# Kernel optimization log

Hardware: AMD Instinct MI355X
Metric: run time of the kernel (lower is better)

Reference implementation:

```python
import jax, jax.numpy as jnp
from jax import lax
import numpy as np

N, C, T, V, P, O = 32, 64, 300, 25, 3, 128
STRIDE = 2
EPS = 1e-5


def setup_inputs() -> dict:
    key = jax.random.key(0)
    ks = jax.random.split(key, 8)
    x = jax.random.normal(ks[0], (N, C, T, V), jnp.float32)
    A_parts = jax.random.uniform(ks[1], (P, V, V), jnp.float32)
    edge_importance = jnp.ones((P,), jnp.float32)
    gcn_w = jax.random.normal(ks[2], (O, C), jnp.float32) * 0.05
    gcn_b = jax.random.normal(ks[3], (O,), jnp.float32) * 0.05
    tcn_w = jax.random.normal(ks[4], (O, O, 9, 1), jnp.float32) * 0.02
    tcn_b = jax.random.normal(ks[5], (O,), jnp.float32) * 0.05
    bn_gamma = jnp.ones((O,), jnp.float32)
    bn_beta = jnp.zeros((O,), jnp.float32)
    res_w = jax.random.normal(ks[6], (O, C), jnp.float32) * 0.05
    res_b = jax.random.normal(ks[7], (O,), jnp.float32) * 0.05
    return {"x": x, "A_parts": A_parts, "edge_importance": edge_importance,
            "gcn_w": gcn_w, "gcn_b": gcn_b, "tcn_w": tcn_w, "tcn_b": tcn_b,
            "bn_gamma": bn_gamma, "bn_beta": bn_beta, "res_w": res_w, "res_b": res_b}


def reference(x, A_parts, edge_importance, gcn_w, gcn_b, tcn_w, tcn_b,
              bn_gamma, bn_beta, res_w, res_b):
    # Fused P-partition aggregation: sum_p (ei_p * A_p) applied once.
    A_sum = jnp.einsum('pvw,p->vw', A_parts, edge_importance)  # [V, V]
    agg = jnp.einsum('nctv,vw->nctw', x, A_sum)                # [N, C, T, V]
    # 1x1 gcn conv == channel matmul
    x_gcn = jnp.einsum('nctv,oc->notv', agg, gcn_w) + gcn_b[None, :, None, None]
    # temporal conv: kernel (9,1), stride (2,1), pad (4,0)
    x_tcn = lax.conv_general_dilated(
        x_gcn, tcn_w, window_strides=(STRIDE, 1), padding=((4, 4), (0, 0)),
        dimension_numbers=('NCHW', 'OIHW', 'NCHW'))
    x_tcn = x_tcn + tcn_b[None, :, None, None]
    # BatchNorm (training mode: batch statistics, biased variance)
    mean = jnp.mean(x_tcn, axis=(0, 2, 3), keepdims=True)
    var = jnp.var(x_tcn, axis=(0, 2, 3), keepdims=True)
    x_bn = (x_tcn - mean) * lax.rsqrt(var + EPS)
    x_bn = x_bn * bn_gamma[None, :, None, None] + bn_beta[None, :, None, None]
    # residual: 1x1 conv, stride (2,1) == temporal subsample + channel matmul
    x_sub = x[:, :, ::STRIDE, :]
    res = jnp.einsum('nctv,oc->notv', x_sub, res_w) + res_b[None, :, None, None]
    return jax.nn.relu(x_bn + res)
```

## Files before the change

kernel.cpp:

```cpp
#include <hip/hip_runtime.h>
#include <hip/hip_bf16.h>

typedef unsigned short u16;
typedef unsigned int   u32;

#define NB 32
#define CC 64
#define TT 300
#define VV 25
#define OO 128
#define TO 150
#define KT 9
#define MM 7500
#define MT 59
#define M2 3750

typedef short s8v  __attribute__((ext_vector_type(8)));
typedef float f4v  __attribute__((ext_vector_type(4)));
typedef u16  h4v  __attribute__((ext_vector_type(4)));
typedef u16  h8v  __attribute__((ext_vector_type(8)));

__device__ __forceinline__ float b2f(u16 u){
  union { u32 i; float f; } c; c.i = ((u32)u) << 16; return c.f;
}
__device__ __forceinline__ u16 f2b(float f){
  __hip_bfloat16 h = __float2bfloat16(f);
  return *reinterpret_cast<u16*>(&h);
}
__device__ __forceinline__ void async16(const void* g, void* l){
  __builtin_amdgcn_global_load_lds((const __attribute__((address_space(1))) u32*)g,
                                   (__attribute__((address_space(3))) u32*)l, 16, 0, 0);
}

__global__ __launch_bounds__(256) void k_prep(const float* __restrict__ Ap, const float* __restrict__ ei,
                                              const float* __restrict__ tw, const float* __restrict__ gw,
                                              const float* __restrict__ rw,
                                              float* __restrict__ Asum, float* __restrict__ zbuf,
                                              u16* __restrict__ Wq2, u16* __restrict__ gwb,
                                              u16* __restrict__ rwb){
  int idx = blockIdx.x * 256 + threadIdx.x;
  if (idx < VV*VV){
    float s = 0.f;
    for (int p = 0; p < 3; ++p) s += ei[p] * Ap[p*VV*VV + idx];
    Asum[idx] = s;
  }
  if (idx >= 640 && idx < 768) zbuf[idx - 640] = 0.f;
  int w = idx - 1024;
  if (w >= 0 && w < 18*OO*64){
    int kc = w >> 13;
    int r  = w & 8191;
    int o  = r >> 6;
    int j  = r & 63;
    int k  = kc >> 1;
    int i  = (kc & 1)*64 + j;
    Wq2[w] = f2b(tw[o*(OO*KT) + i*KT + k]);
  }
  int w2 = idx - 148480;
  if (w2 >= 0 && w2 < OO*CC) gwb[w2] = f2b(gw[w2]);
  int w3 = idx - 156672;
  if (w3 >= 0 && w3 < OO*CC) rwb[w3] = f2b(rw[w3]);
}

__global__ __launch_bounds__(256, 4) void k_gcnm(const float* __restrict__ x, const float* __restrict__ Asum,
                                                 const u16* __restrict__ gwb, const float* __restrict__ gb,
                                                 u16* __restrict__ xg){
  __shared__ __align__(16) u16 A_lds[128*64];
  __shared__ __align__(16) u16 B_lds[128*64];
  int bx = blockIdx.x;
  int n  = bx / MT;
  int m0 = (bx % MT) * 128;
  int t0 = m0 / VV, r0 = m0 % VV;
  int tid = threadIdx.x;
  int lane = tid & 63, wv = tid >> 6;
  int wm = (wv & 1) * 64, wo = (wv >> 1) * 64;
  int lr = lane & 15, lq = lane >> 4;

  {
    const char* gB = (const char*)gwb;
    char* lB = (char*)B_lds;
    #pragma unroll
    for (int i = 0; i < 4; ++i){
      int G = i*256 + tid;
      int row = G >> 3, gp = G & 7;
      int src = (row*8 + (gp ^ (row & 7)))*16;
      async16(gB + src, lB + G*16);
    }
  }

  s8v bfw[2];
  #pragma unroll
  for (int wt = 0; wt < 2; ++wt){
    u16 tmp[8];
    int w = lr + 16*wt;
    #pragma unroll
    for (int j = 0; j < 8; ++j){
      int v = lq*8 + j;
      tmp[j] = (w < VV && v < VV) ? f2b(Asum[v*VV + w]) : (u16)0;
    }
    bfw[wt] = *(s8v*)tmp;
  }

  asm volatile("s_waitcnt vmcnt(0)" ::: "memory");
  __builtin_amdgcn_sched_barrier(0);

  const size_t XTOT = (size_t)NB*CC*TT*VV;
  f4v xa7[7], xb7[7];
  #pragma unroll
  for (int tt = 0; tt < 7; ++tt){
    int tau = tt*4 + wv;
    int it = tau >> 2, ct = tau & 3;
    int t  = t0 + it;
    int c  = ct*16 + lr;
    size_t off = ((size_t)(n*CC + c)*TT + t)*VV + lq*8;
    if (lq == 3) off -= 7;
    if (off > XTOT - 8) off = XTOT - 8;
    const float* xp = x + off;
    asm volatile("global_load_dwordx4 %0, %1, off"            : "=&v"(xa7[tt]) : "v"(xp));
    asm volatile("global_load_dwordx4 %0, %1, off offset:16"  : "=&v"(xb7[tt]) : "v"(xp));
  }

  #pragma unroll
  for (int tt = 0; tt < 7; ++tt){
    if      (tt == 0) asm volatile("s_waitcnt vmcnt(12)" ::: "memory");
    else if (tt == 1) asm volatile("s_waitcnt vmcnt(10)" ::: "memory");
    else if (tt == 2) asm volatile("s_waitcnt vmcnt(8)"  ::: "memory");
    else if (tt == 3) asm volatile("s_waitcnt vmcnt(6)"  ::: "memory");
    else if (tt == 4) asm volatile("s_waitcnt vmcnt(4)"  ::: "memory");
    else if (tt == 5) asm volatile("s_waitcnt vmcnt(2)"  ::: "memory");
    else              asm volatile("s_waitcnt vmcnt(0)"  ::: "memory");
    __builtin_amdgcn_sched_barrier(0);

    int tau = tt*4 + wv;
    int it = tau >> 2, ct = tau & 3;
    int t  = t0 + it;
    bool valid = (t < TT);
    u16 pk[8];
    if (lq < 3){
      if (valid){
        pk[0]=f2b(xa7[tt][0]); pk[1]=f2b(xa7[tt][1]); pk[2]=f2b(xa7[tt][2]); pk[3]=f2b(xa7[tt][3]);
        pk[4]=f2b(xb7[tt][0]); pk[5]=f2b(xb7[tt][1]); pk[6]=f2b(xb7[tt][2]); pk[7]=f2b(xb7[tt][3]);
      } else {
        #pragma unroll
        for (int j = 0; j < 8; ++j) pk[j] = 0;
      }
    } else {
      pk[0] = valid ? f2b(xb7[tt][3]) : (u16)0;
      pk[1]=0; pk[2]=0; pk[3]=0; pk[4]=0; pk[5]=0; pk[6]=0; pk[7]=0;
    }
    s8v af = *(s8v*)pk;
    f4v d0 = (f4v)(0.f), d1 = (f4v)(0.f);
    d0 = __builtin_amdgcn_mfma_f32_16x16x32_bf16(af, bfw[0], d0, 0, 0, 0);
    d1 = __builtin_amdgcn_mfma_f32_16x16x32_bf16(af, bfw[1], d1, 0, 0, 0);
    int cb = ct*16 + lq*4;
    int g  = cb >> 3, co = cb & 7;
    int ml0 = it*VV + lr - r0;
    if (ml0 >= 0 && ml0 < 128){
      u16 q[4];
      #pragma unroll
      for (int rg = 0; rg < 4; ++rg) q[rg] = f2b(d0[rg]);
      *(h4v*)&A_lds[ml0*64 + ((g ^ (ml0 & 7))*8) + co] = *(h4v*)q;
    }
    int w1 = lr + 16;
    int ml1 = it*VV + w1 - r0;
    if (w1 < VV && ml1 >= 0 && ml1 < 128){
      u16 q[4];
      #pragma unroll
      for (int rg = 0; rg < 4; ++rg) q[rg] = f2b(d1[rg]);
      *(h4v*)&A_lds[ml1*64 + ((g ^ (ml1 & 7))*8) + co] = *(h4v*)q;
    }
  }
  __syncthreads();

  f4v acc[4][4];
  #pragma unroll
  for (int mi = 0; mi < 4; ++mi)
    #pragma unroll
    for (int ni = 0; ni < 4; ++ni) acc[mi][ni] = (f4v)(0.f);
  #pragma unroll
  for (int ks = 0; ks < 2; ++ks){
    int p = ((ks*4 + lq) ^ (lane & 7)) * 8;
    s8v af[4], bf[4];
    #pragma unroll
    for (int mi = 0; mi < 4; ++mi)
      af[mi] = *(const s8v*)&A_lds[(wm + mi*16 + lr)*64 + p];
    #pragma unroll
    for (int ni = 0; ni < 4; ++ni)
      bf[ni] = *(const s8v*)&B_lds[(wo + ni*16 + lr)*64 + p];
    #pragma unroll
    for (int mi = 0; mi < 4; ++mi)
      #pragma unroll
      for (int ni = 0; ni < 4; ++ni)
        acc[mi][ni] = __builtin_amdgcn_mfma_f32_16x16x32_bf16(af[mi], bf[ni], acc[mi][ni], 0, 0, 0);
  }

  float bias[4];
  #pragma unroll
  for (int ni = 0; ni < 4; ++ni) bias[ni] = gb[wo + ni*16 + lr];
  #pragma unroll
  for (int mi = 0; mi < 4; ++mi){
    int mr = m0 + wm + mi*16 + lq*4;
    #pragma unroll
    for (int ni = 0; ni < 4; ++ni){
      int o = wo + ni*16 + lr;
      #pragma unroll
      for (int rg = 0; rg < 4; ++rg){
        int m = mr + rg;
        if (m < MM)
          xg[((size_t)n*MM + m)*OO + o] = f2b(acc[mi][ni][rg] + bias[ni]);
      }
    }
  }
}

__global__ __launch_bounds__(512, 4) void k_tcnm(const u16* __restrict__ xg, const u16* __restrict__ Wq2,
                                                 const float* __restrict__ tb, const u16* __restrict__ zbuf,
                                                 u16* __restrict__ xt, float* __restrict__ psum,
                                                 float* __restrict__ psq){
  __shared__ __align__(16) u16 A_lds[2][128*64];
  __shared__ __align__(16) u16 B_lds[2][128*64];
  __shared__ float sredS[8][64];
  __shared__ float sredQ[8][64];
  int bx = blockIdx.x;
  int lg = ((bx & 7) * 120) + (bx >> 3);
  int n  = lg / 30;
  int m0 = (lg % 30) * 128;
  int tid = threadIdx.x;
  int lane = tid & 63, wv = tid >> 6;
  int wm = (wv >> 1) * 32, wo = (wv & 1) * 64;
  int lr = lane & 15, lq = lane >> 4;

  int rlow = tid >> 3;
  int gsrc = (tid & 7) ^ (rlow & 7);
  int tid16 = tid * 16;
  int  tbse[2], vr[2]; bool vm[2];
  #pragma unroll
  for (int it = 0; it < 2; ++it){
    int m = m0 + it*64 + rlow;
    vm[it] = (m < M2);
    int t2 = m / VV, v = m - t2*VV;
    tbse[it] = 2*t2 - 4;
    vr[it] = v;
  }
  size_t basen = (size_t)n*MM*OO + (size_t)gsrc*8;

  f4v acc[2][4];
  #pragma unroll
  for (int mi = 0; mi < 2; ++mi)
    #pragma unroll
    for (int ni = 0; ni < 4; ++ni) acc[mi][ni] = (f4v)(0.f);

  auto stage = [&](int kc, int b){
    int k  = kc >> 1;
    int i0 = (kc & 1) * 64;
    const u16* wbase = Wq2 + kc*8192;
    char* Ab = (char*)(&A_lds[b][0]);
    char* Bb = (char*)(&B_lds[b][0]);
    #pragma unroll
    for (int it = 0; it < 2; ++it){
      int t = tbse[it] + k;
      const u16* ga = (vm[it] && t >= 0 && t < TT)
                      ? xg + basen + (size_t)(t*VV + vr[it])*OO + i0
                      : zbuf;
      async16(ga, Ab + it*8192 + tid16);
      async16(wbase + ((it*64 + rlow)*64 + gsrc*8), Bb + it*8192 + tid16);
    }
  };

  stage(0, 0);
  for (int kc = 0; kc < 18; ++kc){
    int cur = kc & 1;
    if (kc < 17){
      stage(kc + 1, cur ^ 1);
      asm volatile("s_waitcnt vmcnt(4)" ::: "memory");
    } else {
      asm volatile("s_waitcnt vmcnt(0)" ::: "memory");
    }
    __builtin_amdgcn_s_barrier();
    asm volatile("" ::: "memory");

    const u16* Ac = &A_lds[cur][0];
    const u16* Bc = &B_lds[cur][0];
    #pragma unroll
    for (int ks = 0; ks < 2; ++ks){
      int p = ((ks*4 + lq) ^ (lane & 7)) * 8;
      s8v af[2], bf[4];
      #pragma unroll
      for (int mi = 0; mi < 2; ++mi)
        af[mi] = *(const s8v*)&Ac[(wm + mi*16 + lr)*64 + p];
      #pragma unroll
      for (int ni = 0; ni < 4; ++ni)
        bf[ni] = *(const s8v*)&Bc[(wo + ni*16 + lr)*64 + p];
      #pragma unroll
      for (int mi = 0; mi < 2; ++mi)
        #pragma unroll
        for (int ni = 0; ni < 4; ++ni)
          acc[mi][ni] = __builtin_amdgcn_mfma_f32_16x16x32_bf16(af[mi], bf[ni], acc[mi][ni], 0, 0, 0);
    }
    asm volatile("s_waitcnt lgkmcnt(0)" ::: "memory");
    __builtin_amdgcn_s_barrier();
    asm volatile("" ::: "memory");
  }

  float bias[4];
  #pragma unroll
  for (int ni = 0; ni < 4; ++ni) bias[ni] = tb[wo + ni*16 + lr];
  float sni[4] = {0.f,0.f,0.f,0.f}, qni[4] = {0.f,0.f,0.f,0.f};
  #pragma unroll
  for (int mi = 0; mi < 2; ++mi){
    int mr = m0 + wm + mi*16 + lq*4;
    #pragma unroll
    for (int ni = 0; ni < 4; ++ni){
      int o = wo + ni*16 + lr;
      #pragma unroll
      for (int rg = 0; rg < 4; ++rg){
        int mm = mr + rg;
        if (mm < M2){
          float val = acc[mi][ni][rg] + bias[ni];
          xt[((size_t)n*M2 + mm)*OO + o] = f2b(val);
          sni[ni] += val;
          qni[ni] += val*val;
        }
      }
    }
  }
  #pragma unroll
  for (int ni = 0; ni < 4; ++ni){
    float s = sni[ni], q = qni[ni];
    s += __shfl_xor(s, 16); s += __shfl_xor(s, 32);
    q += __shfl_xor(q, 16); q += __shfl_xor(q, 32);
    if (lane < 16){
      sredS[wv][ni*16 + lane] = s;
      sredQ[wv][ni*16 + lane] = q;
    }
  }
  __syncthreads();
  if (tid < 128){
    int o = tid, h = o >> 6, lo = o & 63;
    psum[(size_t)lg*128 + o] = (sredS[h][lo] + sredS[h+2][lo]) + (sredS[h+4][lo] + sredS[h+6][lo]);
  } else if (tid < 256){
    int o = tid - 128, h = o >> 6, lo = o & 63;
    psq [(size_t)lg*128 + o] = (sredQ[h][lo] + sredQ[h+2][lo]) + (sredQ[h+4][lo] + sredQ[h+6][lo]);
  }
}

__global__ __launch_bounds__(256) void k_stats2a(const float* __restrict__ psum, const float* __restrict__ psq,
                                                 float* __restrict__ ps2, float* __restrict__ pq2){
  __shared__ float bufS[256], bufQ[256];
  int tid = threadIdx.x, b = blockIdx.x;
  int o = tid & 127, h = tid >> 7;
  float s = 0.f, q = 0.f;
  for (int r = b*16 + h; r < b*16 + 16; r += 2){
    s += psum[(size_t)r*128 + o];
    q += psq [(size_t)r*128 + o];
  }
  bufS[tid] = s; bufQ[tid] = q;
  __syncthreads();
  if (tid < 128){
    ps2[(size_t)b*128 + o] = bufS[tid] + bufS[tid + 128];
    pq2[(size_t)b*128 + o] = bufQ[tid] + bufQ[tid + 128];
  }
}

__global__ __launch_bounds__(256) void k_stats2b(const float* __restrict__ ps2, const float* __restrict__ pq2,
                                                 const float* __restrict__ gamma, const float* __restrict__ beta,
                                                 float* __restrict__ stats){
  __shared__ float bufS[256], bufQ[256];
  int tid = threadIdx.x;
  int o = tid & 127, h = tid >> 7;
  float s = 0.f, q = 0.f;
  for (int b = h; b < 60; b += 2){
    s += ps2[(size_t)b*128 + o];
    q += pq2[(size_t)b*128 + o];
  }
  bufS[tid] = s; bufQ[tid] = q;
  __syncthreads();
  if (tid < 128){
    s = bufS[tid] + bufS[tid + 128];
    q = bufQ[tid] + bufQ[tid + 128];
    const float inv = 1.f / 120000.f;
    float mean = s * inv;
    float var  = q * inv - mean*mean;
    float sc = gamma[o] * rsqrtf(var + 1e-5f);
    stats[o]       = sc;
    stats[128 + o] = beta[o] - mean * sc;
  }
}

__global__ __launch_bounds__(256, 4) void k_resm(const float* __restrict__ x, const u16* __restrict__ rwb,
                                                 const float* __restrict__ rb, const u16* __restrict__ xt,
                                                 const float* __restrict__ stats, float* __restrict__ out){
  __shared__ __align__(16) char smem[64*130*4];
  u16* A_lds = (u16*)smem;
  u16* B_lds = A_lds + 128*64;
  float* tbuf = (float*)smem;
  int bx = blockIdx.x;
  int n  = bx / 30;
  int m0 = (bx % 30) * 128;
  int t20 = m0 / VV, r0 = m0 % VV;
  int tid = threadIdx.x;
  int lane = tid & 63, wv = tid >> 6;
  int wm = (wv & 1) * 64, wo = (wv >> 1) * 64;
  int lr = lane & 15, lq = lane >> 4;

  {
    const u32* g32 = (const u32*)rwb;
    u32* b32 = (u32*)B_lds;
    for (int s = tid; s < 4096; s += 256){
      int row = s >> 5, col = s & 31;
      int g = col >> 2, c2 = col & 3;
      b32[row*32 + ((g ^ (row & 7))*4 + c2)] = g32[s];
    }
  }

  for (int task = tid; task < 8*7*VV; task += 256){
    int cg  = task / (7*VV);
    int rem = task - cg*(7*VV);
    int t2i = rem / VV, v = rem - t2i*VV;
    int t2 = t20 + t2i;
    int ml = t2i*VV + v - r0;
    if (ml >= 0 && ml < 128){
      u16 pk[8];
      if (t2 < TO){
        const float* xp = x + ((size_t)(n*CC + cg*8)*TT + 2*t2)*VV + v;
        #pragma unroll
        for (int cc = 0; cc < 8; ++cc) pk[cc] = f2b(xp[(size_t)cc*(TT*VV)]);
      } else {
        #pragma unroll
        for (int cc = 0; cc < 8; ++cc) pk[cc] = 0;
      }
      *(h8v*)&A_lds[ml*64 + ((cg ^ (ml & 7))*8)] = *(h8v*)pk;
    }
  }
  __syncthreads();

  f4v acc[4][4];
  #pragma unroll
  for (int mi = 0; mi < 4; ++mi)
    #pragma unroll
    for (int ni = 0; ni < 4; ++ni) acc[mi][ni] = (f4v)(0.f);
  #pragma unroll
  for (int ks = 0; ks < 2; ++ks){
    int p = ((ks*4 + lq) ^ (lane & 7)) * 8;
    s8v af[4], bf[4];
    #pragma unroll
    for (int mi = 0; mi < 4; ++mi)
      af[mi] = *(const s8v*)&A_lds[(wm + mi*16 + lr)*64 + p];
    #pragma unroll
    for (int ni = 0; ni < 4; ++ni)
      bf[ni] = *(const s8v*)&B_lds[(wo + ni*16 + lr)*64 + p];
    #pragma unroll
    for (int mi = 0; mi < 4; ++mi)
      #pragma unroll
      for (int ni = 0; ni < 4; ++ni)
        acc[mi][ni] = __builtin_amdgcn_mfma_f32_16x16x32_bf16(af[mi], bf[ni], acc[mi][ni], 0, 0, 0);
  }

  float sc[4], sb[4], rr[4];
  #pragma unroll
  for (int ni = 0; ni < 4; ++ni){
    int o = wo + ni*16 + lr;
    sc[ni] = stats[o]; sb[ni] = stats[128 + o]; rr[ni] = rb[o];
  }

  #pragma unroll
  for (int pass = 0; pass < 2; ++pass){
    __syncthreads();
    if ((wv >> 1) == pass){
      #pragma unroll
      for (int mi = 0; mi < 4; ++mi){
        int mb   = m0 + wm + mi*16 + lq*4;
        int mloc = wm + mi*16 + lq*4;
        #pragma unroll
        for (int ni = 0; ni < 4; ++ni){
          int o    = wo + ni*16 + lr;
          int oloc = ni*16 + lr;
          size_t xb = ((size_t)n*M2 + mb)*OO + o;
          float v2[4];
          #pragma unroll
          for (int rg = 0; rg < 4; ++rg){
            float val = 0.f;
            if (mb + rg < M2)
              val = fmaxf(sc[ni]*b2f(xt[xb + (size_t)rg*OO]) + sb[ni] + acc[mi][ni][rg] + rr[ni], 0.f);
            v2[rg] = val;
          }
          *(float2*)&tbuf[oloc*130 + mloc]     = make_float2(v2[0], v2[1]);
          *(float2*)&tbuf[oloc*130 + mloc + 2] = make_float2(v2[2], v2[3]);
        }
      }
    }
    __syncthreads();
    #pragma unroll
    for (int it = 0; it < 16; ++it){
      int row = it*4 + (tid >> 6);
      int c2  = (tid & 63) * 2;
      int o   = pass*64 + row;
      int mg  = m0 + c2;
      size_t ob = ((size_t)(n*OO + o))*M2 + mg;
      float2 vv = *(float2*)&tbuf[row*130 + c2];
      if (mg + 1 < M2)      *(float2*)&out[ob] = vv;
      else if (mg < M2)     out[ob] = vv.x;
    }
  }
}

extern "C" void kernel_launch(void* const* d_in, const int* in_sizes, int n_in,
                              void* d_out, int out_size, void* d_ws, size_t ws_size,
                              hipStream_t stream) {
  const float* x     = (const float*)d_in[0];
  const float* Ap    = (const float*)d_in[1];
  const float* ei    = (const float*)d_in[2];
  const float* gw    = (const float*)d_in[3];
  const float* gb    = (const float*)d_in[4];
  const float* tw    = (const float*)d_in[5];
  const float* tb    = (const float*)d_in[6];
  const float* gamma = (const float*)d_in[7];
  const float* beta  = (const float*)d_in[8];
  const float* rw    = (const float*)d_in[9];
  const float* rb    = (const float*)d_in[10];
  float* out = (float*)d_out;

  char* ws = (char*)d_ws;
  float* Asum  = (float*)ws;
  float* zbuf  = (float*)(ws + 2560);
  u16*   Wq2   = (u16*)(ws + 4096);
  u16*   gwb   = (u16*)(ws + 299008);
  u16*   rwb   = (u16*)(ws + 315392);
  float* stats = (float*)(ws + 331776);
  float* psum  = (float*)(ws + 333824);
  float* psq   = (float*)(ws + 825344);
  float* ps2   = (float*)(ws + 1316864);
  float* pq2   = (float*)(ws + 1347584);
  u16*   xg    = (u16*)(ws + (2u<<20));
  u16*   xt    = (u16*)(ws + 63537152);

  k_prep   <<<dim3(644),    dim3(256), 0, stream>>>(Ap, ei, tw, gw, rw, Asum, zbuf, Wq2, gwb, rwb);
  k_gcnm   <<<dim3(NB*MT),  dim3(256), 0, stream>>>(x, Asum, gwb, gb, xg);
  k_tcnm   <<<dim3(NB*30),  dim3(512), 0, stream>>>(xg, Wq2, tb, (const u16*)zbuf, xt, psum, psq);
  k_stats2a<<<dim3(60),     dim3(256), 0, stream>>>(psum, psq, ps2, pq2);
  k_stats2b<<<dim3(1),      dim3(256), 0, stream>>>(ps2, pq2, gamma, beta, stats);
  k_resm   <<<dim3(NB*30),  dim3(256), 0, stream>>>(x, rwb, rb, xt, stats, out);
}
```

Baseline: 257.7 us.

## Load temporal-conv A operand directly into registers instead of staging through LDS

The temporal conv GEMM kernel now fetches the activation (A) fragments for each MFMA straight from global memory into double-buffered registers with inline global_load_dwordx4, removing the A tile from LDS. Only the weight (B) tile still goes through async LDS copies. This removes LDS traffic and LDS footprint for A, which may help occupancy. In exchange it raises register pressure, issues narrower per-lane global loads with less coalescing, and waits with vmcnt(0) at every step, which reduces overlap between loads and MFMA work.

```diff
diff --git a/kernel.cpp b/kernel.cpp
--- a/kernel.cpp
+++ b/kernel.cpp
@@ -212,11 +212,26 @@
   }
 }
 
+#define TCN_ISSUE(KC, SET) do {                                                         \
+    const u16* wbase_ = Wq2 + (KC)*8192;                                                \
+    char* Bb_ = (char*)(&B_lds[SET][0]);                                                \
+    async16(wbase_ + (0*64 + rlow)*64 + gsrc*8, Bb_ + 0*8192 + tid16);                  \
+    async16(wbase_ + (1*64 + rlow)*64 + gsrc*8, Bb_ + 1*8192 + tid16);                  \
+    _Pragma("unroll")                                                                   \
+    for (int mi_ = 0; mi_ < 2; ++mi_){                                                  \
+      int t_ = tb_[mi_] + ((KC) >> 1);                                                  \
+      bool val_ = mv_[mi_] && (t_ >= 0) && (t_ < TT);                                   \
+      const u16* p_ = val_ ? (xgn + (size_t)(t_*VV + vv_[mi_])*OO + ((KC)&1)*64 + jo)   \
+                           : (zbuf + jo);                                               \
+      asm volatile("global_load_dwordx4 %0, %1, off"           : "=&v"(aR[SET][mi_*2+0]) : "v"(p_)); \
+      asm volatile("global_load_dwordx4 %0, %1, off offset:64" : "=&v"(aR[SET][mi_*2+1]) : "v"(p_)); \
+    }                                                                                   \
+  } while(0)
+
 __global__ __launch_bounds__(512, 4) void k_tcnm(const u16* __restrict__ xg, const u16* __restrict__ Wq2,
                                                  const float* __restrict__ tb, const u16* __restrict__ zbuf,
                                                  u16* __restrict__ xt, float* __restrict__ psum,
                                                  float* __restrict__ psq){
-  __shared__ __align__(16) u16 A_lds[2][128*64];
   __shared__ __align__(16) u16 B_lds[2][128*64];
   __shared__ float sredS[8][64];
   __shared__ float sredQ[8][64];
@@ -232,16 +247,18 @@
   int rlow = tid >> 3;
   int gsrc = (tid & 7) ^ (rlow & 7);
   int tid16 = tid * 16;
-  int  tbse[2], vr[2]; bool vm[2];
-  #pragma unroll
-  for (int it = 0; it < 2; ++it){
-    int m = m0 + it*64 + rlow;
-    vm[it] = (m < M2);
-    int t2 = m / VV, v = m - t2*VV;
-    tbse[it] = 2*t2 - 4;
-    vr[it] = v;
-  }
-  size_t basen = (size_t)n*MM*OO + (size_t)gsrc*8;
+
+  int tb_[2], vv_[2]; bool mv_[2];
+  #pragma unroll
+  for (int mi = 0; mi < 2; ++mi){
+    int m_ = m0 + wm + mi*16 + lr;
+    mv_[mi] = (m_ < M2);
+    int t2 = m_ / VV, v = m_ - t2*VV;
+    tb_[mi] = 2*t2 - 4;
+    vv_[mi] = v;
+  }
+  const u16* xgn = xg + (size_t)n*MM*OO;
+  int jo = lq*8;
 
   f4v acc[2][4];
   #pragma unroll
@@ -249,44 +266,27 @@
     #pragma unroll
     for (int ni = 0; ni < 4; ++ni) acc[mi][ni] = (f4v)(0.f);
 
-  auto stage = [&](int kc, int b){
-    int k  = kc >> 1;
-    int i0 = (kc & 1) * 64;
-    const u16* wbase = Wq2 + kc*8192;
-    char* Ab = (char*)(&A_lds[b][0]);
-    char* Bb = (char*)(&B_lds[b][0]);
-    #pragma unroll
-    for (int it = 0; it < 2; ++it){
-      int t = tbse[it] + k;
-      const u16* ga = (vm[it] && t >= 0 && t < TT)
-                      ? xg + basen + (size_t)(t*VV + vr[it])*OO + i0
-                      : zbuf;
-      async16(ga, Ab + it*8192 + tid16);
-      async16(wbase + ((it*64 + rlow)*64 + gsrc*8), Bb + it*8192 + tid16);
-    }
-  };
-
-  stage(0, 0);
+  s8v aR[2][4];
+
+  TCN_ISSUE(0, 0);
+
+  #pragma unroll
   for (int kc = 0; kc < 18; ++kc){
-    int cur = kc & 1;
-    if (kc < 17){
-      stage(kc + 1, cur ^ 1);
-      asm volatile("s_waitcnt vmcnt(4)" ::: "memory");
-    } else {
-      asm volatile("s_waitcnt vmcnt(0)" ::: "memory");
-    }
+    asm volatile("s_waitcnt vmcnt(0)" ::: "memory");
+    __builtin_amdgcn_sched_barrier(0);
     __builtin_amdgcn_s_barrier();
     asm volatile("" ::: "memory");
 
-    const u16* Ac = &A_lds[cur][0];
-    const u16* Bc = &B_lds[cur][0];
+    if (kc < 17){
+      if ((kc & 1) == 0) TCN_ISSUE(kc+1, 1);
+      else               TCN_ISSUE(kc+1, 0);
+    }
+
+    const u16* Bc = &B_lds[kc & 1][0];
     #pragma unroll
     for (int ks = 0; ks < 2; ++ks){
       int p = ((ks*4 + lq) ^ (lane & 7)) * 8;
-      s8v af[2], bf[4];
-      #pragma unroll
-      for (int mi = 0; mi < 2; ++mi)
-        af[mi] = *(const s8v*)&Ac[(wm + mi*16 + lr)*64 + p];
+      s8v bf[4];
       #pragma unroll
       for (int ni = 0; ni < 4; ++ni)
         bf[ni] = *(const s8v*)&Bc[(wo + ni*16 + lr)*64 + p];
@@ -294,7 +294,7 @@
       for (int mi = 0; mi < 2; ++mi)
         #pragma unroll
         for (int ni = 0; ni < 4; ++ni)
-          acc[mi][ni] = __builtin_amdgcn_mfma_f32_16x16x32_bf16(af[mi], bf[ni], acc[mi][ni], 0, 0, 0);
+          acc[mi][ni] = __builtin_amdgcn_mfma_f32_16x16x32_bf16(aR[kc & 1][mi*2+ks], bf[ni], acc[mi][ni], 0, 0, 0);
     }
     asm volatile("s_waitcnt lgkmcnt(0)" ::: "memory");
     __builtin_amdgcn_s_barrier();
```

New measurement: 293.7 us. +13.9%, slower.
